# Kernel optimization log

Hardware: AMD Instinct MI355X
Metric: run time of the kernel (lower is better)

The kernel has to match this reference:

```python
import jax, jax.numpy as jnp
import numpy as np

D_MODEL = 1024
N_HEADS = 16
D_HEAD = D_MODEL // N_HEADS
D_FF = 4096
BATCH = 2
SEQ = 2048
EPS = 1e-5


def setup_inputs() -> dict:
    key = jax.random.key(0)
    ks = jax.random.split(key, 8)
    s = 0.02
    x = jax.random.normal(ks[0], (BATCH, SEQ, D_MODEL), dtype=jnp.float32)
    # Per-head projection weights, stacked: [H, d_head, d_model] (torch Linear stores (out,in))
    wq = jax.random.normal(ks[1], (N_HEADS, D_HEAD, D_MODEL), dtype=jnp.float32) * s
    wk = jax.random.normal(ks[2], (N_HEADS, D_HEAD, D_MODEL), dtype=jnp.float32) * s
    wv = jax.random.normal(ks[3], (N_HEADS, D_HEAD, D_MODEL), dtype=jnp.float32) * s
    wo = jax.random.normal(ks[4], (D_MODEL, D_MODEL), dtype=jnp.float32) * s
    w1 = jax.random.normal(ks[5], (D_FF, D_MODEL), dtype=jnp.float32) * s
    w2 = jax.random.normal(ks[6], (D_MODEL, D_FF), dtype=jnp.float32) * s
    ln1_g = jnp.ones((D_MODEL,), jnp.float32)
    ln1_b = jnp.zeros((D_MODEL,), jnp.float32)
    ln2_g = jnp.ones((D_MODEL,), jnp.float32)
    ln2_b = jnp.zeros((D_MODEL,), jnp.float32)
    return {"x": x, "wq": wq, "wk": wk, "wv": wv, "wo": wo,
            "w1": w1, "w2": w2, "ln1_g": ln1_g, "ln1_b": ln1_b,
            "ln2_g": ln2_g, "ln2_b": ln2_b}


def _layer_norm(x, g, b):
    mu = jnp.mean(x, axis=-1, keepdims=True)
    var = jnp.mean(jnp.square(x - mu), axis=-1, keepdims=True)
    return (x - mu) * jax.lax.rsqrt(var + EPS) * g + b


def _mha(h, wq, wk, wv, wo):
    # h: [b,s,d]; wq/wk/wv: [H,dh,d] -> q/k/v: [b,H,s,dh]
    q = jnp.einsum('bsd,hed->bhse', h, wq)
    k = jnp.einsum('bsd,hed->bhse', h, wk)
    v = jnp.einsum('bsd,hed->bhse', h, wv)
    scores = jnp.einsum('bhqe,bhke->bhqk', q, k) / jnp.sqrt(jnp.float32(D_HEAD))
    weights = jax.nn.softmax(scores, axis=-1)
    ctx = jnp.einsum('bhqk,bhke->bhqe', weights, v)  # [b,H,s,dh]
    # concat heads in order (head 0 first) -> [b,s,H*dh]
    concat = jnp.transpose(ctx, (0, 2, 1, 3)).reshape(h.shape[0], h.shape[1], D_MODEL)
    return concat @ wo.T


def reference(x, wq, wk, wv, wo, w1, w2, ln1_g, ln1_b, ln2_g, ln2_b):
    h = _layer_norm(x, ln1_g, ln1_b)
    attn_out = _mha(h, wq, wk, wv, wo)
    h2 = _layer_norm(x + attn_out, ln2_g, ln2_b)
    ff = jax.nn.gelu(h2 @ w1.T, approximate=False) @ w2.T
    return x + ff
```

## Files before the change

kernel.cpp:

```cpp
#include <hip/hip_runtime.h>
#include <hip/hip_bf16.h>
#include <math.h>

typedef __bf16 bf16_t;
typedef __bf16 bf16x8 __attribute__((ext_vector_type(8)));
typedef __bf16 bf16x4 __attribute__((ext_vector_type(4)));
typedef float f32x4 __attribute__((ext_vector_type(4)));
typedef unsigned int u32;
typedef u32 u32x2 __attribute__((ext_vector_type(2)));

#define DM 1024
#define SEQL 2048
#define NTOK 4096
#define QKVN 3072

__device__ __forceinline__ void gload_lds16(const bf16_t* g, bf16_t* l){
  __builtin_amdgcn_global_load_lds((const __attribute__((address_space(1))) void*)g,
                                   (__attribute__((address_space(3))) void*)l, 16, 0, 0);
}
__device__ __forceinline__ u32 ldsoff(const void* p){
  return (u32)(size_t)(__attribute__((address_space(3))) const void*)p;
}
__device__ __forceinline__ u32x2 tr64(u32 byte_off){
  u32x2 d;
  asm volatile("ds_read_b64_tr_b16 %0, %1" : "=v"(d) : "v"(byte_off));
  return d;
}
__device__ __forceinline__ u32 pack2(float a, float b){
  union{ __bf16 h[2]; u32 w; } z;
  z.h[0]=(__bf16)a; z.h[1]=(__bf16)b; return z.w;
}

__global__ __launch_bounds__(256) void prep_kernel(
    const float* __restrict__ wq, const float* __restrict__ wk,
    const float* __restrict__ wv, const float* __restrict__ wo,
    const float* __restrict__ w1, const float* __restrict__ w2,
    const float* __restrict__ x,  const float* __restrict__ g1,
    const float* __restrict__ b1,
    bf16_t* __restrict__ wqkv_b, bf16_t* __restrict__ wo_b,
    bf16_t* __restrict__ w1_b,   bf16_t* __restrict__ w2_b,
    bf16_t* __restrict__ h1)
{
  __shared__ float red[8];
  const int bid = blockIdx.x;
  const int t = threadIdx.x;
  if (bid < 12288){
    const int flat = (bid*256 + t)*4;
    const int seg = flat >> 20;
    const int off1m = flat & 1048575;
    const float* src; bf16_t* dst;
    if (seg < 3){
      src = (seg==0 ? wq : (seg==1 ? wk : wv)) + off1m;
      dst = wqkv_b + flat;
    } else if (seg == 3){
      src = wo + off1m;  dst = wo_b + off1m;
    } else if (seg < 8){
      src = w1 + (flat - 4*1048576);  dst = w1_b + (flat - 4*1048576);
    } else {
      src = w2 + (flat - 8*1048576);  dst = w2_b + (flat - 8*1048576);
    }
    const float4 v = *(const float4*)src;
    bf16x4 o; o[0]=(__bf16)v.x; o[1]=(__bf16)v.y; o[2]=(__bf16)v.z; o[3]=(__bf16)v.w;
    *(bf16x4*)dst = o;
  } else {
    const int row = bid - 12288;
    const float4 v = *(const float4*)(x + (size_t)row*DM + t*4);
    float s  = v.x+v.y+v.z+v.w;
    float sq = v.x*v.x+v.y*v.y+v.z*v.z+v.w*v.w;
    #pragma unroll
    for (int m=1;m<64;m<<=1){ s += __shfl_xor(s,m); sq += __shfl_xor(sq,m); }
    const int w = t>>6;
    if ((t&63)==0){ red[w]=s; red[4+w]=sq; }
    __syncthreads();
    s  = red[0]+red[1]+red[2]+red[3];
    sq = red[4]+red[5]+red[6]+red[7];
    const float mean = s*(1.f/DM);
    const float var  = sq*(1.f/DM) - mean*mean;
    const float rstd = rsqrtf(var + 1e-5f);
    const float4 gg = *(const float4*)(g1 + t*4);
    const float4 bb = *(const float4*)(b1 + t*4);
    bf16x4 o;
    o[0]=(__bf16)((v.x-mean)*rstd*gg.x+bb.x);
    o[1]=(__bf16)((v.y-mean)*rstd*gg.y+bb.y);
    o[2]=(__bf16)((v.z-mean)*rstd*gg.z+bb.z);
    o[3]=(__bf16)((v.w-mean)*rstd*gg.w+bb.w);
    *(bf16x4*)(h1 + (size_t)row*DM + t*4) = o;
  }
}

__global__ __launch_bounds__(256) void lnb_kernel(const bf16_t* __restrict__ in,
    const float* __restrict__ g, const float* __restrict__ bta,
    bf16_t* __restrict__ outp)
{
  const int row = blockIdx.x;
  const int t = threadIdx.x;
  const bf16x4 raw = *(const bf16x4*)(in + (size_t)row*DM + t*4);
  float4 v;
  v.x=(float)raw[0]; v.y=(float)raw[1]; v.z=(float)raw[2]; v.w=(float)raw[3];
  float s  = v.x+v.y+v.z+v.w;
  float sq = v.x*v.x+v.y*v.y+v.z*v.z+v.w*v.w;
  #pragma unroll
  for (int m=1;m<64;m<<=1){ s += __shfl_xor(s,m); sq += __shfl_xor(sq,m); }
  __shared__ float red[8];
  const int w = t>>6;
  if ((t&63)==0){ red[w]=s; red[4+w]=sq; }
  __syncthreads();
  s  = red[0]+red[1]+red[2]+red[3];
  sq = red[4]+red[5]+red[6]+red[7];
  const float mean = s*(1.f/DM);
  const float var  = sq*(1.f/DM) - mean*mean;
  const float rstd = rsqrtf(var + 1e-5f);
  const float4 gg = *(const float4*)(g + t*4);
  const float4 bb = *(const float4*)(bta + t*4);
  bf16x4 o;
  o[0]=(__bf16)((v.x-mean)*rstd*gg.x+bb.x);
  o[1]=(__bf16)((v.y-mean)*rstd*gg.y+bb.y);
  o[2]=(__bf16)((v.z-mean)*rstd*gg.z+bb.z);
  o[3]=(__bf16)((v.w-mean)*rstd*gg.w+bb.w);
  *(bf16x4*)(outp + (size_t)row*DM + t*4) = o;
}

__global__ __launch_bounds__(256) void red4_kernel(
    const bf16_t* __restrict__ p0, const bf16_t* __restrict__ p1,
    const bf16_t* __restrict__ p2, const bf16_t* __restrict__ p3,
    const float* __restrict__ x, float* __restrict__ outp)
{
  const int i = (blockIdx.x*256 + threadIdx.x)*4;
  const bf16x4 a0 = *(const bf16x4*)(p0 + i);
  const bf16x4 a1 = *(const bf16x4*)(p1 + i);
  const bf16x4 a2 = *(const bf16x4*)(p2 + i);
  const bf16x4 a3 = *(const bf16x4*)(p3 + i);
  const float4 xs = *(const float4*)(x + i);
  float4 o;
  o.x = xs.x + ((float)a0[0]+(float)a1[0]) + ((float)a2[0]+(float)a3[0]);
  o.y = xs.y + ((float)a0[1]+(float)a1[1]) + ((float)a2[1]+(float)a3[1]);
  o.z = xs.z + ((float)a0[2]+(float)a1[2]) + ((float)a2[2]+(float)a3[2]);
  o.w = xs.w + ((float)a0[3]+(float)a1[3]) + ((float)a2[3]+(float)a3[3]);
  *(float4*)(outp + i) = o;
}

template<int EPI>
__global__ __launch_bounds__(512, 2) void gemm8ph(
    const bf16_t* __restrict__ A, const bf16_t* __restrict__ Bw,
    void* __restrict__ c0, void* __restrict__ c1,
    void* __restrict__ c2, void* __restrict__ c3,
    int N, int K, int lda)
{
  __shared__ __align__(16) char ldsb[131072];
  const int tid = threadIdx.x, lane = tid&63, wid = tid>>6;
  const int q16 = lane&15, g = lane>>4;
  const int wm = wid>>2, wn = wid&3;

  const int flat = blockIdx.y*gridDim.x + blockIdx.x;
  const int xcd = flat&7, jj = flat>>3;
  const int NY = gridDim.y;
  const int jdiv = jj/NY, jmod = jj - jdiv*NY;
  const int bm = (xcd*2 + jdiv)*256, bn = jmod*256;
  const int sk = blockIdx.z;
  const int koff = sk*K;
  void* Cout = (sk==0) ? c0 : (sk==1) ? c1 : (sk==2) ? c2 : c3;

  int mloc, kloc;
  {
    const u32 L = tid*16;
    const u32 logical = L ^ (((L>>9)&1)<<5);
    mloc = (int)(logical>>6);
    kloc = (int)((logical&63)>>1);
  }
  const bf16_t* asrc = A  + (size_t)(bm + mloc)*lda + koff + kloc;
  const bf16_t* bsrc = Bw + (size_t)(bn + mloc)*lda + koff + kloc;
  const u32 laneOff = ((u32)(q16*64 + g*16)) ^ ((u32)(q16&8)<<2);

  f32x4 acc[8][4] = {};
  bf16x8 bv[4];

  auto stage = [&](int buf, int kh, int isB, int s){
    const bf16_t* src = isB ? bsrc : asrc;
    #pragma unroll
    for (int h2=0; h2<2; h2++)
      gload_lds16(src + (size_t)(h2*128)*lda + s*64 + kh*32,
                  (bf16_t*)(ldsb + buf*65536 + isB*32768 + kh*16384 + h2*8192 + tid*16));
  };

  stage(0,0,0,0); stage(0,0,1,0); stage(0,1,0,0); stage(0,1,1,0);
  stage(1,0,0,1); stage(1,0,1,1);
  asm volatile("s_waitcnt vmcnt(4)" ::: "memory");
  __builtin_amdgcn_s_barrier();

  const int NSTEP = K>>6;
  const int NIT = NSTEP>>1;

#define PHASE(BUF,KH,MH,DOST,SBUF,SKH,SISB,SSTEP,CK) { \
    bf16x8 av[4]; \
    const char* Ab_ = ldsb + (BUF)*65536 + (KH)*16384 + wm*8192; \
    _Pragma("unroll") for (int jx=0;jx<4;jx++) \
      av[jx] = *(const bf16x8*)(Ab_ + (((MH)*4+jx)<<10) + laneOff); \
    if ((MH)==0){ \
      const char* Bb_ = ldsb + (BUF)*65536 + 32768 + (KH)*16384 + (wn>>1)*8192; \
      _Pragma("unroll") for (int jx=0;jx<4;jx++) \
        bv[jx] = *(const bf16x8*)(Bb_ + ((((wn&1)*4)+jx)<<10) + laneOff); \
    } \
    if (DOST) stage(SBUF,SKH,SISB,SSTEP); \
    asm volatile("s_barrier" ::: "memory"); \
    asm volatile("s_waitcnt lgkmcnt(0)" ::: "memory"); \
    __builtin_amdgcn_s_setprio(1); \
    _Pragma("unroll") for (int jx=0;jx<4;jx++) \
      _Pragma("unroll") for (int j2=0;j2<4;j2++) \
        acc[(MH)*4+jx][j2] = __builtin_amdgcn_mfma_f32_16x16x32_bf16(av[jx], bv[j2], acc[(MH)*4+jx][j2],0,0,0); \
    __builtin_amdgcn_s_setprio(0); \
    if (CK){ if (nl) { asm volatile("s_waitcnt vmcnt(4)" ::: "memory"); } \
             else    { asm volatile("s_waitcnt vmcnt(0)" ::: "memory"); } } \
    asm volatile("s_barrier" ::: "memory"); }

  for (int it=0; it<NIT; it++){
    const int s0 = 2*it, s1 = s0+1;
    const bool nl = (it+1 < NIT);
    PHASE(0,0,0, 1,  1,1,0, s1,   0)
    PHASE(0,0,1, 1,  1,1,1, s1,   0)
    PHASE(0,1,0, nl, 0,0,0, s0+2, 0)
    PHASE(0,1,1, nl, 0,0,1, s0+2, 1)
    PHASE(1,0,0, nl, 0,1,0, s0+2, 0)
    PHASE(1,0,1, nl, 0,1,1, s0+2, 0)
    PHASE(1,1,0, nl, 1,0,0, s1+2, 0)
    PHASE(1,1,1, nl, 1,0,1, s1+2, 1)
  }
#undef PHASE

  #pragma unroll
  for (int fm=0; fm<8; fm++)
    #pragma unroll
    for (int fn=0; fn<4; fn++)
      #pragma unroll
      for (int i=0; i<4; i++){
        const int r = bm + wm*128 + fm*16 + g*4 + i;
        const int c = bn + wn*64 + fn*16 + q16;
        const size_t idx = (size_t)r*N + c;
        const float vv = acc[fm][fn][i];
        if constexpr (EPI==0){
          ((bf16_t*)Cout)[idx] = (__bf16)vv;
        } else {
          const float ge = 0.5f*vv*(1.0f + erff(vv*0.70710678118654752f));
          ((bf16_t*)Cout)[idx] = (__bf16)ge;
        }
      }
}

template<int EPI>
__global__ __launch_bounds__(512, 2) void gemm128(
    const bf16_t* __restrict__ A, const bf16_t* __restrict__ Bw,
    void* __restrict__ Cout, const float* __restrict__ X,
    int N, int K)
{
  constexpr int BK = 32;
  __shared__ __align__(16) char ldsb[3*16384];
  const int tid = threadIdx.x, lane = tid&63, wid = tid>>6;
  const int q16 = lane&15, g = lane>>4;
  const int wm = wid>>2, wn = wid&3;

  const int flat = blockIdx.y*gridDim.x + blockIdx.x;
  const int xcd = flat&7, j = flat>>3;
  const int bm = ((xcd<<2) + (j>>3))*128, bn = (j&7)*128;

  int mloc, kloc;
  {
    const u32 L = tid*16;
    const u32 logical = L ^ (((L>>9)&1)<<5);
    mloc = (int)(logical>>6);
    kloc = (int)((logical&63)>>1);
  }
  const bf16_t* asrc = A  + (size_t)(bm + mloc)*K + kloc;
  const bf16_t* bsrc = Bw + (size_t)(bn + mloc)*K + kloc;
  const u32 laneOff = ((u32)(q16*64 + g*16)) ^ ((u32)(q16&8)<<2);

  f32x4 acc[4][2] = {};

  auto stageA = [&](int buf, int k0){
    gload_lds16(asrc + k0, (bf16_t*)(ldsb + buf*16384 + tid*16));
  };
  auto stageB = [&](int buf, int k0){
    gload_lds16(bsrc + k0, (bf16_t*)(ldsb + buf*16384 + 8192 + tid*16));
  };

  stageA(0,0); stageB(0,0);
  stageA(1,BK); stageB(1,BK);
  asm volatile("s_waitcnt vmcnt(2)" ::: "memory");
  __builtin_amdgcn_s_barrier();

  const int NT = K/BK;
  int bcur = 0;
  for (int kt=0; kt<NT; kt++){
    const int bstg = (bcur >= 1) ? bcur-1 : bcur+2;
    const char* Ab = ldsb + bcur*16384 + wm*4096;
    const char* Bb = ldsb + bcur*16384 + 8192 + wn*2048;
    const bool sOK = (kt+2 < NT);
    const int k0s = (kt+2)*BK;
    bf16x8 bv[2];
    #pragma unroll
    for (int p=0; p<2; p++){
      bf16x8 av[2];
      #pragma unroll
      for (int jx=0;jx<2;jx++)
        av[jx] = *(const bf16x8*)(Ab + ((p*2+jx)<<10) + laneOff);
      if (p==0){
        #pragma unroll
        for (int jx=0;jx<2;jx++)
          bv[jx] = *(const bf16x8*)(Bb + (jx<<10) + laneOff);
      }
      if (sOK){
        if (p==0) stageA(bstg,k0s);
        else      stageB(bstg,k0s);
      }
      asm volatile("s_barrier" ::: "memory");
      __builtin_amdgcn_s_setprio(1);
      #pragma unroll
      for (int jx=0;jx<2;jx++)
        #pragma unroll
        for (int j2=0;j2<2;j2++)
          acc[p*2+jx][j2] = __builtin_amdgcn_mfma_f32_16x16x32_bf16(av[jx], bv[j2], acc[p*2+jx][j2], 0,0,0);
      __builtin_amdgcn_s_setprio(0);
      if (p==1){
        if (sOK) asm volatile("s_waitcnt vmcnt(2)" ::: "memory");
        else     asm volatile("s_waitcnt vmcnt(0)" ::: "memory");
      }
      asm volatile("s_barrier" ::: "memory");
    }
    bcur = (bcur==2)?0:bcur+1;
  }

  #pragma unroll
  for (int fm=0; fm<4; fm++)
    #pragma unroll
    for (int fn=0; fn<2; fn++)
      #pragma unroll
      for (int i=0; i<4; i++){
        const int r = bm + wm*64 + fm*16 + g*4 + i;
        const int c = bn + wn*32 + fn*16 + q16;
        const size_t idx = (size_t)r*N + c;
        const float vv = X[idx] + acc[fm][fn][i];
        ((bf16_t*)Cout)[idx] = (__bf16)vv;
      }
}

__global__ __launch_bounds__(512, 4) void attn_kernel(
    const bf16_t* __restrict__ QKV, bf16_t* __restrict__ Ctx)
{
  __shared__ __align__(16) bf16_t Ks[2][128*64];
  __shared__ __align__(16) bf16_t Vs[2][32*4*72];
  const int tid = threadIdx.x, lane = tid&63, w = tid>>6;
  const int g = lane>>4, q16 = lane&15;
  const int bh = blockIdx.y, b = bh>>4, h = bh&15;
  const int qr0 = blockIdx.x*128 + w*16;
  const size_t tok0 = (size_t)b*SEQL;
  const int ch0 = h*64;

  bf16x8 aq[2];
  #pragma unroll
  for (int ks=0; ks<2; ks++){
    bf16x8 t = *(const bf16x8*)(QKV + (tok0+qr0+q16)*QKVN + ch0 + ks*32 + g*8);
    #pragma unroll
    for (int jx=0;jx<8;jx++) t[jx] = (__bf16)((float)t[jx]*0.18033688f);
    aq[ks] = t;
  }

  const int srow = tid>>3, sc8 = (tid&7)*8;
  const bf16_t* kptr_swz = QKV + (tok0+srow)*QKVN + 1024 + ch0 + (sc8 ^ ((srow&7)<<3));
  const bf16_t* vptr = QKV + (tok0+srow)*QKVN + 2048 + ch0 + sc8;
  const int vwoff = ((srow>>2)*4 + (sc8>>4))*72 + (srow&3)*16 + (sc8&15);

  float mrun = -1e30f, lrun = 0.f;
  f32x4 o[4] = {};

  #pragma unroll
  for (int it=0; it<2; it++)
    gload_lds16(kptr_swz + (size_t)(it*64)*QKVN, &Ks[0][tid*8 + it*4096]);
  bf16x8 vreg[2];
  #pragma unroll
  for (int it=0; it<2; it++)
    vreg[it] = *(const bf16x8*)(vptr + (size_t)(it*64)*QKVN);
  #pragma unroll
  for (int it=0; it<2; it++)
    *(bf16x8*)&Vs[0][vwoff + it*4608] = vreg[it];
  #pragma unroll
  for (int it=0; it<2; it++)
    vreg[it] = *(const bf16x8*)(vptr + (size_t)(128 + it*64)*QKVN);

  const int NT = SEQL/128;
  for (int t=0; t<NT; t++){
    __syncthreads();
    if (t+1 < NT){
      #pragma unroll
      for (int it=0; it<2; it++){
        gload_lds16(kptr_swz + (size_t)((t+1)*128 + it*64)*QKVN, &Ks[(t+1)&1][tid*8 + it*4096]);
        *(bf16x8*)&Vs[(t+1)&1][vwoff + it*4608] = vreg[it];
      }
      if (t+2 < NT){
        #pragma unroll
        for (int it=0; it<2; it++)
          vreg[it] = *(const bf16x8*)(vptr + (size_t)((t+2)*128 + it*64)*QKVN);
      }
    }
    const bf16_t* ksb = Ks[t&1];
    const u32 vs0 = ldsoff(&Vs[t&1][0]);

    f32x4 s[8] = {};
    #pragma unroll
    for (int ks=0; ks<2; ks++){
      #pragma unroll
      for (int fn=0; fn<8; fn++){
        const int r = fn*16 + q16;
        const int ce = ks*32 + g*8;
        bf16x8 bk = *(const bf16x8*)&ksb[r*64 + (ce ^ ((r&7)<<3))];
        s[fn] = __builtin_amdgcn_mfma_f32_16x16x32_bf16(bk, aq[ks], s[fn], 0, 0, 0);
      }
    }

    float mx = -1e30f;
    #pragma unroll
    for (int fn=0; fn<8; fn++)
      mx = fmaxf(mx, fmaxf(fmaxf(s[fn][0],s[fn][1]), fmaxf(s[fn][2],s[fn][3])));
    mx = fmaxf(mx, __shfl_xor(mx,16));
    mx = fmaxf(mx, __shfl_xor(mx,32));

    if (!__all(mx <= mrun + 11.54f)){
      const float mnew = fmaxf(mrun, mx);
      const float alpha = __builtin_amdgcn_exp2f(mrun - mnew);
      #pragma unroll
      for (int i=0;i<4;i++){
        const float ai = __shfl(alpha, g*4+i);
        o[0][i]*=ai; o[1][i]*=ai; o[2][i]*=ai; o[3][i]*=ai;
      }
      lrun *= alpha;
      mrun = mnew;
    }

    float rs = 0.f;
    u32 u[8][2];
    #pragma unroll
    for (int fn=0; fn<8; fn++){
      const float e0=__builtin_amdgcn_exp2f(s[fn][0]-mrun);
      const float e1=__builtin_amdgcn_exp2f(s[fn][1]-mrun);
      const float e2=__builtin_amdgcn_exp2f(s[fn][2]-mrun);
      const float e3=__builtin_amdgcn_exp2f(s[fn][3]-mrun);
      rs += (e0+e1)+(e2+e3);
      u[fn][0] = pack2(e0,e1);
      u[fn][1] = pack2(e2,e3);
    }
    rs += __shfl_xor(rs,16);
    rs += __shfl_xor(rs,32);
    lrun += rs;

    #pragma unroll
    for (int ks=0; ks<4; ks++){
      u32x2 vlo[4], vhi[4];
      #pragma unroll
      for (int ne=0; ne<4; ne++){
        const u32 vb = vs0 + (u32)((((ks*8 + 2*g)*4 + ne)*72 + q16)*2);
        vlo[ne] = tr64(vb);
        vhi[ne] = tr64(vb + 576);
      }
      union { u32 wd[4]; bf16x8 v; } pa;
      #pragma unroll
      for (int jj=0; jj<4; jj++){
        const int src = q16 + ((((g&1)<<1) + (jj>>1))<<4);
        const u32 a0 = (u32)__shfl((int)u[2*ks  ][jj&1], src);
        const u32 a1 = (u32)__shfl((int)u[2*ks+1][jj&1], src);
        pa.wd[jj] = (g&2) ? a1 : a0;
      }
      asm volatile("s_waitcnt lgkmcnt(0)" ::: "memory");
      __builtin_amdgcn_sched_barrier(0);
      union { u32x2 u2[2]; bf16x8 v; } cc;
      #pragma unroll
      for (int ne=0; ne<4; ne++){
        cc.u2[0]=vlo[ne]; cc.u2[1]=vhi[ne];
        o[ne] = __builtin_amdgcn_mfma_f32_16x16x32_bf16(pa.v, cc.v, o[ne], 0, 0, 0);
      }
    }
  }

  const float rl = 1.0f/lrun;
  #pragma unroll
  for (int i=0; i<4; i++){
    const float ri = __shfl(rl, g*4+i);
    #pragma unroll
    for (int ne=0; ne<4; ne++){
      const int r = qr0 + g*4 + i;
      Ctx[(tok0+r)*DM + ch0 + ne*16 + q16] = (__bf16)(o[ne][i]*ri);
    }
  }
}

extern "C" void kernel_launch(void* const* d_in, const int* in_sizes, int n_in,
                              void* d_out, int out_size, void* d_ws, size_t ws_size,
                              hipStream_t stream)
{
  (void)in_sizes; (void)n_in; (void)out_size; (void)ws_size;
  const float* x  = (const float*)d_in[0];
  const float* wq = (const float*)d_in[1];
  const float* wk = (const float*)d_in[2];
  const float* wv = (const float*)d_in[3];
  const float* wo = (const float*)d_in[4];
  const float* w1 = (const float*)d_in[5];
  const float* w2 = (const float*)d_in[6];
  const float* g1 = (const float*)d_in[7];
  const float* b1 = (const float*)d_in[8];
  const float* g2 = (const float*)d_in[9];
  const float* b2 = (const float*)d_in[10];
  float* out = (float*)d_out;
  char* ws = (char*)d_ws;
  const size_t MB = 1024ull*1024ull;

  bf16_t* wqkv_b = (bf16_t*)(ws);
  bf16_t* wo_b   = (bf16_t*)(ws + 6*MB);
  bf16_t* w1_b   = (bf16_t*)(ws + 8*MB);
  bf16_t* w2_b   = (bf16_t*)(ws + 16*MB);
  bf16_t* h1     = (bf16_t*)(ws + 24*MB);
  bf16_t* qkv    = (bf16_t*)(ws + 32*MB);
  bf16_t* ctx    = (bf16_t*)(ws + 56*MB);
  bf16_t* res2b  = (bf16_t*)(ws + 64*MB);
  bf16_t* h2     = h1;
  bf16_t* ffm    = (bf16_t*)(ws + 32*MB);
  bf16_t* p0     = (bf16_t*)(ws);
  bf16_t* p1     = (bf16_t*)(ws + 8*MB);
  bf16_t* p2     = (bf16_t*)(ws + 24*MB);
  bf16_t* p3     = (bf16_t*)(ws + 64*MB);

  prep_kernel<<<16384, 256, 0, stream>>>(wq, wk, wv, wo, w1, w2, x, g1, b1,
                                         wqkv_b, wo_b, w1_b, w2_b, h1);
  gemm8ph<0><<<dim3(16, 12), 512, 0, stream>>>(h1, wqkv_b, (void*)qkv, (void*)qkv,
                                               (void*)qkv, (void*)qkv, QKVN, 1024, 1024);
  attn_kernel<<<dim3(16, 32), 512, 0, stream>>>(qkv, ctx);
  gemm128<0><<<dim3(32, 8), 512, 0, stream>>>(ctx, wo_b, (void*)res2b, x, 1024, 1024);
  lnb_kernel<<<NTOK, 256, 0, stream>>>(res2b, g2, b2, h2);
  gemm8ph<2><<<dim3(16, 16), 512, 0, stream>>>(h2, w1_b, (void*)ffm, (void*)ffm,
                                               (void*)ffm, (void*)ffm, 4096, 1024, 1024);
  gemm8ph<0><<<dim3(16, 4, 4), 512, 0, stream>>>(ffm, w2_b, (void*)p0, (void*)p1,
                                                 (void*)p2, (void*)p3, 1024, 1024, 4096);
  red4_kernel<<<4096, 256, 0, stream>>>(p0, p1, p2, p3, x, out);
}
```

Baseline: 244.1 us.

## Use tanh-approximate GELU and double-buffer V transpose reads in attention PV loop

Replaces the exact erf-based GELU in the FFN GEMM epilogue with a tanh approximation built from exp2 and a hardware reciprocal, which is cheaper per element. Separately, the attention PV loop now double-buffers the transposed V LDS reads, issuing the next k-step's reads before waiting only on the current ones so LDS latency overlaps with MFMA. The GELU change departs from the exact erf form the reference specifies, which risks tolerance differences. The partial lgkmcnt waits must match the number of outstanding shuffle and LDS operations to stay correct.

```diff
diff --git a/kernel.cpp b/kernel.cpp
--- a/kernel.cpp
+++ b/kernel.cpp
@@ -29,6 +29,14 @@
 __device__ __forceinline__ u32 pack2(float a, float b){
   union{ __bf16 h[2]; u32 w; } z;
   z.h[0]=(__bf16)a; z.h[1]=(__bf16)b; return z.w;
+}
+__device__ __forceinline__ float gelu_fast(float x){
+  const float y = 0.79788456f*(x + 0.044715f*x*x*x);
+  float a = y*2.885390082f;
+  a = fminf(fmaxf(a, -30.f), 30.f);
+  const float t = __builtin_amdgcn_exp2f(a);
+  const float th = (t-1.0f)*__builtin_amdgcn_rcpf(t+1.0f);
+  return 0.5f*x*(1.0f+th);
 }
 
 __global__ __launch_bounds__(256) void prep_kernel(
@@ -239,8 +247,7 @@
         if constexpr (EPI==0){
           ((bf16_t*)Cout)[idx] = (__bf16)vv;
         } else {
-          const float ge = 0.5f*vv*(1.0f + erff(vv*0.70710678118654752f));
-          ((bf16_t*)Cout)[idx] = (__bf16)ge;
+          ((bf16_t*)Cout)[idx] = (__bf16)gelu_fast(vv);
         }
       }
 }
@@ -449,30 +456,46 @@
     rs += __shfl_xor(rs,32);
     lrun += rs;
 
-    #pragma unroll
-    for (int ks=0; ks<4; ks++){
-      u32x2 vlo[4], vhi[4];
+    {
+      u32x2 loA[4], hiA[4], loB[4], hiB[4];
       #pragma unroll
       for (int ne=0; ne<4; ne++){
-        const u32 vb = vs0 + (u32)((((ks*8 + 2*g)*4 + ne)*72 + q16)*2);
-        vlo[ne] = tr64(vb);
-        vhi[ne] = tr64(vb + 576);
-      }
-      union { u32 wd[4]; bf16x8 v; } pa;
-      #pragma unroll
-      for (int jj=0; jj<4; jj++){
-        const int src = q16 + ((((g&1)<<1) + (jj>>1))<<4);
-        const u32 a0 = (u32)__shfl((int)u[2*ks  ][jj&1], src);
-        const u32 a1 = (u32)__shfl((int)u[2*ks+1][jj&1], src);
-        pa.wd[jj] = (g&2) ? a1 : a0;
-      }
-      asm volatile("s_waitcnt lgkmcnt(0)" ::: "memory");
-      __builtin_amdgcn_sched_barrier(0);
-      union { u32x2 u2[2]; bf16x8 v; } cc;
-      #pragma unroll
-      for (int ne=0; ne<4; ne++){
-        cc.u2[0]=vlo[ne]; cc.u2[1]=vhi[ne];
-        o[ne] = __builtin_amdgcn_mfma_f32_16x16x32_bf16(pa.v, cc.v, o[ne], 0, 0, 0);
+        const u32 vb = vs0 + (u32)(((2*g*4 + ne)*72 + q16)*2);
+        loA[ne] = tr64(vb);
+        hiA[ne] = tr64(vb + 576);
+      }
+      #pragma unroll
+      for (int ks=0; ks<4; ks++){
+        union { u32 wd[4]; bf16x8 v; } pa;
+        #pragma unroll
+        for (int jj=0; jj<4; jj++){
+          const int src = q16 + ((((g&1)<<1) + (jj>>1))<<4);
+          const u32 a0 = (u32)__shfl((int)u[2*ks  ][jj&1], src);
+          const u32 a1 = (u32)__shfl((int)u[2*ks+1][jj&1], src);
+          pa.wd[jj] = (g&2) ? a1 : a0;
+        }
+        if (ks < 3){
+          u32x2* nl_ = (ks&1) ? loA : loB;
+          u32x2* nh_ = (ks&1) ? hiA : hiB;
+          #pragma unroll
+          for (int ne=0; ne<4; ne++){
+            const u32 vb = vs0 + (u32)(((((ks+1)*8 + 2*g)*4 + ne)*72 + q16)*2);
+            nl_[ne] = tr64(vb);
+            nh_[ne] = tr64(vb + 576);
+          }
+          asm volatile("s_waitcnt lgkmcnt(8)" ::: "memory");
+        } else {
+          asm volatile("s_waitcnt lgkmcnt(0)" ::: "memory");
+        }
+        __builtin_amdgcn_sched_barrier(0);
+        const u32x2* lo = (ks&1) ? loB : loA;
+        const u32x2* hi = (ks&1) ? hiB : hiA;
+        union { u32x2 u2[2]; bf16x8 v; } cc;
+        #pragma unroll
+        for (int ne=0; ne<4; ne++){
+          cc.u2[0]=lo[ne]; cc.u2[1]=hi[ne];
+          o[ne] = __builtin_amdgcn_mfma_f32_16x16x32_bf16(pa.v, cc.v, o[ne], 0, 0, 0);
+        }
       }
     }
   }
```

New measurement: 233.0 us. 4.5% less time.
